# Kernel optimization log

Hardware: AMD Instinct MI355X
Metric: run time of the kernel (lower is better)

Reference implementation:

```python
import jax, jax.numpy as jnp
import numpy as np

N_NODES = 100000
N_EDGES = 1600000
F_IN = 128
D_OUT = 64
BN_EPS = 1e-3  # keras BatchNormalization default epsilon
LRELU_SLOPE = 0.2  # tf.nn.leaky_relu default alpha


def setup_inputs() -> dict:
    key = jax.random.key(0)
    ks = jax.random.split(key, 6)
    x = jax.random.normal(ks[0], (N_NODES, F_IN), dtype=jnp.float32)
    src = jax.random.randint(ks[1], (N_EDGES,), 0, N_NODES, dtype=jnp.int32)
    dst = jax.random.randint(ks[2], (N_EDGES,), 0, N_NODES, dtype=jnp.int32)
    adj_vals = jnp.ones((N_EDGES,), dtype=jnp.float32)
    W = jax.random.normal(ks[3], (F_IN, D_OUT), dtype=jnp.float32)
    K1 = jax.random.normal(ks[4], (F_IN, F_IN), dtype=jnp.float32)
    K2 = jax.random.normal(ks[5], (F_IN, F_IN), dtype=jnp.float32)
    return {"x": x, "src": src, "dst": dst, "adj_vals": adj_vals, "W": W, "K1": K1, "K2": K2}


def reference(x, src, dst, adj_vals, W, K1, K2):
    n = x.shape[0]
    # training-mode batch norm over the node (batch) axis, gamma=1, beta=0
    mean = jnp.mean(x, axis=0)
    var = jnp.var(x, axis=0)
    xn = (x - mean) * jax.lax.rsqrt(var + BN_EPS)
    mapped = xn @ W                                   # [N, D]
    a1 = jnp.tanh(jnp.sum((xn @ K1) * xn, axis=1))    # [N] row scalar
    a2 = jnp.tanh(jnp.sum((xn @ K2) * xn, axis=1))    # [N] col scalar
    # edge score e_ij = leaky_relu(v_ij*a1[i] + v_ij*a2[j])
    e = jax.nn.leaky_relu(adj_vals * (a1[src] + a2[dst]), negative_slope=LRELU_SLOPE)
    # per-row (src) sparse softmax
    emax = jax.ops.segment_max(e, src, num_segments=n)
    ee = jnp.exp(e - emax[src])
    denom = jax.ops.segment_sum(ee, src, num_segments=n)
    attn = ee / denom[src]                            # [E]
    # SpMM: out[i] = sum_j attn_ij * mapped[j]
    out = jax.ops.segment_sum(attn[:, None] * mapped[dst], src, num_segments=n)
    return jnp.tanh(out)
```

## Files before the change

### kernel.cpp

```cpp
#include <hip/hip_runtime.h>
#include <hip/hip_fp16.h>
#include <math.h>

#define F_IN 128
#define D_OUT 64
#define LRELU 0.2f
#define BN_EPS 1e-3f
#define XPITCH 136
#define NB 391
#define CHA 2048
#define CAPB 6144

typedef __attribute__((ext_vector_type(8))) __bf16 bf16x8;
typedef __attribute__((ext_vector_type(4))) __bf16 bf16x4;
typedef __attribute__((ext_vector_type(4))) float f32x4;

__global__ __launch_bounds__(256) void stats_kernel(const float* __restrict__ x,
                                                    float* __restrict__ sum,
                                                    float* __restrict__ sumsq,
                                                    int N, int rowsPerBlock) {
    __shared__ float lsum[8][132], lsq[8][132];
    int tid  = threadIdx.x;
    int c4   = (tid & 31) * 4;
    int rgrp = tid >> 5;
    int rbeg = blockIdx.x * rowsPerBlock;
    int rend = min(rbeg + rowsPerBlock, N);
    float sx = 0.f, sy = 0.f, sz = 0.f, sw = 0.f;
    float qx = 0.f, qy = 0.f, qz = 0.f, qw = 0.f;
    for (int r = rbeg + rgrp; r < rend; r += 8) {
        float4 v = *(const float4*)&x[(size_t)r * F_IN + c4];
        sx += v.x; sy += v.y; sz += v.z; sw += v.w;
        qx += v.x * v.x; qy += v.y * v.y; qz += v.z * v.z; qw += v.w * v.w;
    }
    lsum[rgrp][c4] = sx; lsum[rgrp][c4 + 1] = sy;
    lsum[rgrp][c4 + 2] = sz; lsum[rgrp][c4 + 3] = sw;
    lsq[rgrp][c4] = qx; lsq[rgrp][c4 + 1] = qy;
    lsq[rgrp][c4 + 2] = qz; lsq[rgrp][c4 + 3] = qw;
    __syncthreads();
    if (tid < 128) {
        float a = 0.f, b = 0.f;
#pragma unroll
        for (int g = 0; g < 8; ++g) { a += lsum[g][tid]; b += lsq[g][tid]; }
        atomicAdd(&sum[tid], a);
        atomicAdd(&sumsq[tid], b);
    }
}

__global__ void finalize_stats(float* sum, float* sumsq, int N) {
    int c = threadIdx.x;
    float mean = sum[c] / (float)N;
    float var  = sumsq[c] / (float)N - mean * mean;
    sum[c]   = mean;
    sumsq[c] = rsqrtf(var + BN_EPS);
}

__global__ __launch_bounds__(256) void prep_B(const float* __restrict__ K1,
                                              const float* __restrict__ K2,
                                              const float* __restrict__ W,
                                              __bf16* __restrict__ Bth,
                                              __bf16* __restrict__ Btl) {
    int i = blockIdx.x * 256 + threadIdx.x;
    if (i >= 320 * 128) return;
    int c = i >> 7, k = i & 127;
    float v;
    if (c < 128)      v = K1[k * 128 + c];
    else if (c < 256) v = K2[k * 128 + (c - 128)];
    else              v = W[k * 64 + (c - 256)];
    __bf16 h = (__bf16)v;
    int ct = c >> 4, col16 = c & 15;
    int ks = k >> 5, quad = (k >> 3) & 3, e = k & 7;
    int off = ct * 2048 + ks * 512 + (quad * 16 + col16) * 8 + e;
    Bth[off] = h;
    Btl[off] = (__bf16)(v - (float)h);
}

__global__ __launch_bounds__(256, 2) void node_kernel(const float* __restrict__ x,
                                                      const __bf16* __restrict__ Bth,
                                                      const __bf16* __restrict__ Btl,
                                                      const float* __restrict__ meanv,
                                                      const float* __restrict__ rstdv,
                                                      float* __restrict__ a1,
                                                      float* __restrict__ a2,
                                                      __half* __restrict__ mapped,
                                                      int N) {
    __shared__ __bf16 xh[64][XPITCH];
    __shared__ __bf16 xl[64][XPITCH];
    __shared__ float mS[128], rS[128];
    __shared__ float paA[4][64], paB[4][64];

    int tid   = threadIdx.x;
    int lane  = tid & 63;
    int w     = tid >> 6;
    int col16 = lane & 15;
    int quad  = lane >> 4;
    int kb    = quad * 8;

    if (tid < 128) { mS[tid] = meanv[tid]; rS[tid] = rstdv[tid]; }
    __syncthreads();

    int base = blockIdx.x * 64;

#pragma unroll
    for (int it = 0; it < 8; ++it) {
        int chunk = tid + it * 256;
        int r = chunk >> 5, c4 = (chunk & 31) * 4;
        int row = base + r;
        float f0 = 0.f, f1 = 0.f, f2 = 0.f, f3 = 0.f;
        if (row < N) {
            float4 v  = *(const float4*)&x[(size_t)row * F_IN + c4];
            float4 m  = *(const float4*)&mS[c4];
            float4 rs = *(const float4*)&rS[c4];
            f0 = (v.x - m.x) * rs.x; f1 = (v.y - m.y) * rs.y;
            f2 = (v.z - m.z) * rs.z; f3 = (v.w - m.w) * rs.w;
        }
        __bf16 h0 = (__bf16)f0, h1 = (__bf16)f1, h2 = (__bf16)f2, h3 = (__bf16)f3;
        bf16x4 hv = {h0, h1, h2, h3};
        bf16x4 lv = {(__bf16)(f0 - (float)h0), (__bf16)(f1 - (float)h1),
                     (__bf16)(f2 - (float)h2), (__bf16)(f3 - (float)h3)};
        *(bf16x4*)&xh[r][c4] = hv;
        *(bf16x4*)&xl[r][c4] = lv;
    }
    __syncthreads();

    float pa1[4] = {0, 0, 0, 0}, pa2[4] = {0, 0, 0, 0};

#pragma unroll
    for (int i = 0; i < 5; ++i) {
        int ct = w * 5 + i;
        const __bf16* ph = Bth + ct * 2048 + lane * 8;
        const __bf16* pl = Btl + ct * 2048 + lane * 8;
        bf16x8 Bh[4], Bl[4];
#pragma unroll
        for (int ks = 0; ks < 4; ++ks) {
            Bh[ks] = *(const bf16x8*)(ph + ks * 512);
            Bl[ks] = *(const bf16x8*)(pl + ks * 512);
        }
        bool isK  = (ct < 16);
        bool isA1 = (ct < 8);
        int cg = (ct & 7) * 16 + quad * 4;
        int cw = (ct - 16) * 16 + quad * 4;
#pragma unroll
        for (int rt = 0; rt < 4; ++rt) {
            int arow = rt * 16 + col16;
            bf16x8 Ah[4], Al[4];
#pragma unroll
            for (int ks = 0; ks < 4; ++ks) {
                Ah[ks] = *(bf16x8*)&xh[arow][ks * 32 + kb];
                Al[ks] = *(bf16x8*)&xl[arow][ks * 32 + kb];
            }
            f32x4 accA = {0, 0, 0, 0}, accB = {0, 0, 0, 0}, accC = {0, 0, 0, 0};
#pragma unroll
            for (int ks = 0; ks < 4; ++ks) {
                accA = __builtin_amdgcn_mfma_f32_16x16x32_bf16(Bh[ks], Ah[ks], accA, 0, 0, 0);
                accB = __builtin_amdgcn_mfma_f32_16x16x32_bf16(Bh[ks], Al[ks], accB, 0, 0, 0);
                accC = __builtin_amdgcn_mfma_f32_16x16x32_bf16(Bl[ks], Ah[ks], accC, 0, 0, 0);
            }
            f32x4 accT = accA + accB + accC;
            if (isK) {
                bf16x4 xh4 = *(bf16x4*)&xh[arow][cg];
                bf16x4 xl4 = *(bf16x4*)&xl[arow][cg];
                float s = accT[0] * ((float)xh4[0] + (float)xl4[0])
                        + accT[1] * ((float)xh4[1] + (float)xl4[1])
                        + accT[2] * ((float)xh4[2] + (float)xl4[2])
                        + accT[3] * ((float)xh4[3] + (float)xl4[3]);
                if (isA1) pa1[rt] += s; else pa2[rt] += s;
            } else {
                int node = base + arow;
                if (node < N) {
                    __half2 h01 = __floats2half2_rn(accT[0], accT[1]);
                    __half2 h23 = __floats2half2_rn(accT[2], accT[3]);
                    __half2* mp = (__half2*)&mapped[(size_t)node * 64 + cw];
                    mp[0] = h01; mp[1] = h23;
                }
            }
        }
    }

#pragma unroll
    for (int rt = 0; rt < 4; ++rt) {
        float v1 = pa1[rt], v2 = pa2[rt];
        v1 += __shfl_xor(v1, 16, 64); v1 += __shfl_xor(v1, 32, 64);
        v2 += __shfl_xor(v2, 16, 64); v2 += __shfl_xor(v2, 32, 64);
        if (quad == 0) {
            paA[w][rt * 16 + col16] = v1;
            paB[w][rt * 16 + col16] = v2;
        }
    }
    __syncthreads();
    if (tid < 64) {
        int node = base + tid;
        if (node < N) {
            a1[node] = tanhf(paA[0][tid] + paA[1][tid] + paA[2][tid] + paA[3][tid]);
            a2[node] = tanhf(paB[0][tid] + paB[1][tid] + paB[2][tid] + paB[3][tid]);
        }
    }
}

__global__ __launch_bounds__(256) void bhist_kernel(const int* __restrict__ src,
                                                    int* __restrict__ partial, int E) {
    __shared__ int h[NB];
    for (int b = threadIdx.x; b < NB; b += 256) h[b] = 0;
    __syncthreads();
    int beg = blockIdx.x * CHA;
    int end = min(beg + CHA, E);
    for (int e = beg + threadIdx.x; e < end; e += 256)
        atomicAdd(&h[src[e] >> 8], 1);
    __syncthreads();
    for (int b = threadIdx.x; b < NB; b += 256)
        partial[blockIdx.x * NB + b] = h[b];
}

__global__ __launch_bounds__(256) void bscan2_kernel(const int* __restrict__ partial,
                                                     int* __restrict__ baseT,
                                                     int* __restrict__ btot,
                                                     int nblkA) {
    __shared__ int tsum[256];
    int b   = blockIdx.x;
    int tid = threadIdx.x;
    int per = (nblkA + 255) / 256;
    int lv[8];
    int r0 = tid * per;
    int mysum = 0;
    for (int i = 0; i < per; ++i) {
        int r = r0 + i;
        lv[i] = (r < nblkA) ? partial[r * NB + b] : 0;
        mysum += lv[i];
    }
    tsum[tid] = mysum;
    for (int off = 1; off < 256; off <<= 1) {
        __syncthreads();
        int t = (tid >= off) ? tsum[tid - off] : 0;
        __syncthreads();
        tsum[tid] += t;
    }
    __syncthreads();
    int run = tsum[tid] - mysum;
    for (int i = 0; i < per; ++i) {
        int r = r0 + i;
        if (r < nblkA) { baseT[r * NB + b] = run; run += lv[i]; }
    }
    if (tid == 255) btot[b] = tsum[255];
}

__global__ __launch_bounds__(512) void bscan_kernel(const int* __restrict__ btot,
                                                    int* __restrict__ bscan,
                                                    int* __restrict__ rowptr,
                                                    int N, int E) {
    __shared__ int s[512];
    int b = threadIdx.x;
    int v = (b < NB) ? btot[b] : 0;
    s[b] = v;
    for (int off = 1; off < 512; off <<= 1) {
        __syncthreads();
        int t = (b >= off) ? s[b - off] : 0;
        __syncthreads();
        s[b] += t;
    }
    __syncthreads();
    if (b < NB) bscan[b] = s[b] - v;
    if (b == 0) { bscan[NB] = E; rowptr[N] = E; }
}

__global__ __launch_bounds__(256) void binA_kernel(const int* __restrict__ src,
                                                   const int* __restrict__ dst,
                                                   const float* __restrict__ adj,
                                                   const float* __restrict__ a1,
                                                   const float* __restrict__ a2,
                                                   const int* __restrict__ partial,
                                                   const int* __restrict__ baseT,
                                                   const int* __restrict__ bscan,
                                                   int2* __restrict__ sorted, int E) {
    __shared__ int2 listL[CHA];
    __shared__ int  addrL[CHA];
    __shared__ int  scan0[NB], scanW[NB], curL[NB];
    __shared__ int  tsum[256];
    int tid = threadIdx.x;
    int blk = blockIdx.x;
    int ebase = blk * CHA;
    int count = min(CHA, E - ebase);

    int b0 = tid * 2, b1 = tid * 2 + 1;
    int v0 = (b0 < NB) ? partial[blk * NB + b0] : 0;
    int v1 = (b1 < NB) ? partial[blk * NB + b1] : 0;
    tsum[tid] = v0 + v1;
    for (int off = 1; off < 256; off <<= 1) {
        __syncthreads();
        int t = (tid >= off) ? tsum[tid - off] : 0;
        __syncthreads();
        tsum[tid] += t;
    }
    __syncthreads();
    int excl = tsum[tid] - v0 - v1;
    if (b0 < NB) {
        scan0[b0] = excl; scanW[b0] = excl;
        curL[b0] = baseT[blk * NB + b0] + bscan[b0];
    }
    if (b1 < NB) {
        scan0[b1] = excl + v0; scanW[b1] = excl + v0;
        curL[b1] = baseT[blk * NB + b1] + bscan[b1];
    }
    __syncthreads();

    for (int i = tid; i < count; i += 256) {
        int e = ebase + i;
        int s = src[e], d = dst[e];
        float v = adj[e] * (a1[s] + a2[d]);
        v = (v > 0.f) ? v : LRELU * v;
        float ex = __expf(v);
        int b = s >> 8;
        int p = atomicAdd(&scanW[b], 1);
        listL[p] = make_int2(((s & 255) << 24) | d, __float_as_int(ex));
        addrL[p] = curL[b] + (p - scan0[b]);
    }
    __syncthreads();
    for (int i = tid; i < count; i += 256)
        sorted[addrL[i]] = listL[i];
}

__global__ __launch_bounds__(256) void binB_kernel(const int* __restrict__ bscan,
                                                   int2* __restrict__ sorted,
                                                   int* __restrict__ rowptr, int N) {
    __shared__ int2 inL[CAPB];
    __shared__ int2 outL[CAPB];
    __shared__ int  c0[257], cW[256];
    int b   = blockIdx.x;
    int lo  = b << 8;
    int bbase = bscan[b];
    int len   = bscan[b + 1] - bbase;
    len = min(len, CAPB);
    int tid = threadIdx.x;
    cW[tid] = 0;
    __syncthreads();
    for (int i = tid; i < len; i += 256) {
        int2 pe = sorted[bbase + i];
        inL[i] = pe;
        atomicAdd(&cW[((unsigned)pe.x) >> 24], 1);
    }
    __syncthreads();
    if (tid == 0) {
        int run = 0;
        for (int k = 0; k < 256; ++k) { int c = cW[k]; c0[k] = run; run += c; }
    }
    __syncthreads();
    if (lo + tid < N) rowptr[lo + tid] = bbase + c0[tid];
    cW[tid] = c0[tid];
    __syncthreads();
    for (int i = tid; i < len; i += 256) {
        int2 pe = inL[i];
        unsigned u = (unsigned)pe.x;
        int p = atomicAdd(&cW[u >> 24], 1);
        outL[p] = make_int2((int)(u & 0xFFFFFF), pe.y);
    }
    __syncthreads();
    for (int i = tid; i < len; i += 256)
        sorted[bbase + i] = outL[i];
}

#define SPMM_ACC(P, G)                                        \
    {                                                         \
        float wg = __int_as_float(P.y);                       \
        accw += wg;                                           \
        float2 m0 = __half22float2(*(__half2*)&G.x);          \
        float2 m1 = __half22float2(*(__half2*)&G.y);          \
        float2 m2 = __half22float2(*(__half2*)&G.z);          \
        float2 m3 = __half22float2(*(__half2*)&G.w);          \
        acc0 += wg * m0.x; acc1 += wg * m0.y;                 \
        acc2 += wg * m1.x; acc3 += wg * m1.y;                 \
        acc4 += wg * m2.x; acc5 += wg * m2.y;                 \
        acc6 += wg * m3.x; acc7 += wg * m3.y;                 \
    }

__global__ __launch_bounds__(256) void spmm_kernel(const int* __restrict__ rowptr,
                                                   const int2* __restrict__ sorted,
                                                   const __half2* __restrict__ mapped,
                                                   float* __restrict__ out, int N) {
    __shared__ float accL[8][64];
    __shared__ float accwL[8];
    int tid  = threadIdx.x;
    int w    = tid >> 6;
    int lane = tid & 63;
    int half = lane >> 5;
    int slot = (lane >> 3) & 3;
    int c    = lane & 7;
    int nl   = w * 2 + half;
    int node = blockIdx.x * 8 + nl;
    int beg = 0, end = 0;
    if (node < N) { beg = rowptr[node]; end = rowptr[node + 1]; }

    float acc0 = 0.f, acc1 = 0.f, acc2 = 0.f, acc3 = 0.f;
    float acc4 = 0.f, acc5 = 0.f, acc6 = 0.f, acc7 = 0.f;
    float accw = 0.f;
    const char* mb = (const char*)mapped;

    for (int chunk = beg; chunk < end; chunk += 16) {
        int e0 = chunk + slot;
        int2 p0 = (e0      < end) ? sorted[e0]      : make_int2(0, 0);
        int2 p1 = (e0 + 4  < end) ? sorted[e0 + 4]  : make_int2(0, 0);
        int2 p2 = (e0 + 8  < end) ? sorted[e0 + 8]  : make_int2(0, 0);
        int2 p3 = (e0 + 12 < end) ? sorted[e0 + 12] : make_int2(0, 0);
        int4 g0 = *(const int4*)(mb + (((unsigned)p0.x << 7) | (c << 4)));
        int4 g1 = *(const int4*)(mb + (((unsigned)p1.x << 7) | (c << 4)));
        int4 g2 = *(const int4*)(mb + (((unsigned)p2.x << 7) | (c << 4)));
        int4 g3 = *(const int4*)(mb + (((unsigned)p3.x << 7) | (c << 4)));
        SPMM_ACC(p0, g0);
        SPMM_ACC(p1, g1);
        SPMM_ACC(p2, g2);
        SPMM_ACC(p3, g3);
    }

#pragma unroll
    for (int off = 8; off < 32; off <<= 1) {
        acc0 += __shfl_xor(acc0, off, 64);
        acc1 += __shfl_xor(acc1, off, 64);
        acc2 += __shfl_xor(acc2, off, 64);
        acc3 += __shfl_xor(acc3, off, 64);
        acc4 += __shfl_xor(acc4, off, 64);
        acc5 += __shfl_xor(acc5, off, 64);
        acc6 += __shfl_xor(acc6, off, 64);
        acc7 += __shfl_xor(acc7, off, 64);
        accw += __shfl_xor(accw, off, 64);
    }
    if (slot == 0) {
        float* al = &accL[nl][c * 8];
        al[0] = acc0; al[1] = acc1; al[2] = acc2; al[3] = acc3;
        al[4] = acc4; al[5] = acc5; al[6] = acc6; al[7] = acc7;
        if (c == 0) accwL[nl] = accw;
    }
    __syncthreads();

    int n    = tid >> 5;
    int col  = tid & 31;
    int node2 = blockIdx.x * 8 + n;
    if (node2 < N) {
        float aw  = accwL[n];
        float inv = (aw != 0.f) ? 1.f / aw : 0.f;
        float* op = &out[(size_t)node2 * 64];
        op[col]      = tanhf(accL[n][col] * inv);
        op[col + 32] = tanhf(accL[n][col + 32] * inv);
    }
}

extern "C" void kernel_launch(void* const* d_in, const int* in_sizes, int n_in,
                              void* d_out, int out_size, void* d_ws, size_t ws_size,
                              hipStream_t stream) {
    const float* x   = (const float*)d_in[0];
    const int*   src = (const int*)d_in[1];
    const int*   dst = (const int*)d_in[2];
    const float* adj = (const float*)d_in[3];
    const float* W   = (const float*)d_in[4];
    const float* K1  = (const float*)d_in[5];
    const float* K2  = (const float*)d_in[6];
    float* out = (float*)d_out;

    const int N = in_sizes[0] / F_IN;
    const int E = in_sizes[1];
    const int nblkA = (E + CHA - 1) / CHA;

    float* meanv  = (float*)d_ws;
    float* rstdv  = meanv + 128;
    float* a1     = rstdv + 128;
    float* a2     = a1 + N;
    __half* mapped = (__half*)(a2 + N);
    int*   rowptr = (int*)(mapped + (size_t)N * 64);
    int*   bscan  = rowptr + (N + 1);
    int*   btot   = bscan + (NB + 1);
    int*   partial = btot + NB;
    int*   baseT   = partial + (size_t)nblkA * NB;
    uintptr_t sp  = ((uintptr_t)(baseT + (size_t)nblkA * NB) + 15) & ~(uintptr_t)15;
    int2*  sorted = (int2*)sp;
    __bf16* Bth   = (__bf16*)(sorted + E);
    __bf16* Btl   = Bth + 320 * 128;

    hipMemsetAsync(d_ws, 0, 256 * sizeof(float), stream);

    bhist_kernel<<<nblkA, 256, 0, stream>>>(src, partial, E);

    int rpb = (N + 511) / 512;
    stats_kernel<<<512, 256, 0, stream>>>(x, meanv, rstdv, N, rpb);
    finalize_stats<<<1, 128, 0, stream>>>(meanv, rstdv, N);

    prep_B<<<(320 * 128 + 255) / 256, 256, 0, stream>>>(K1, K2, W, Bth, Btl);

    node_kernel<<<(N + 63) / 64, 256, 0, stream>>>(x, Bth, Btl, meanv, rstdv,
                                                   a1, a2, mapped, N);

    bscan2_kernel<<<NB, 256, 0, stream>>>(partial, baseT, btot, nblkA);
    bscan_kernel<<<1, 512, 0, stream>>>(btot, bscan, rowptr, N, E);

    binA_kernel<<<nblkA, 256, 0, stream>>>(src, dst, adj, a1, a2,
                                           partial, baseT, bscan, sorted, E);
    binB_kernel<<<NB, 256, 0, stream>>>(bscan, sorted, rowptr, N);

    spmm_kernel<<<(N + 7) / 8, 256, 0, stream>>>(rowptr, sorted,
                                                 (const __half2*)mapped, out, N);
}
```

Measured before the change: 284.3 us.

## Double node tile to 128 rows and reuse A fragments across two column tiles

The node kernel now processes 128 nodes per block instead of 64. Each wave loads B fragments for two column tiles at once and reuses every loaded A row fragment across both, so LDS reads of A are halved and B global loads are amortized over more rows. In exchange LDS use roughly doubles to about 70KB per block and register pressure rises from the doubled B fragments and the accumulators. Occupancy may drop below the launch-bounds target of 2 blocks, and the grid has half as many blocks.

```diff
diff --git a/kernel.cpp b/kernel.cpp
--- a/kernel.cpp
+++ b/kernel.cpp
@@ -83,10 +83,10 @@
                                                       float* __restrict__ a2,
                                                       __half* __restrict__ mapped,
                                                       int N) {
-    __shared__ __bf16 xh[64][XPITCH];
-    __shared__ __bf16 xl[64][XPITCH];
+    __shared__ __bf16 xh[128][XPITCH];
+    __shared__ __bf16 xl[128][XPITCH];
     __shared__ float mS[128], rS[128];
-    __shared__ float paA[4][64], paB[4][64];
+    __shared__ float paA[4][128], paB[4][128];
 
     int tid   = threadIdx.x;
     int lane  = tid & 63;
@@ -98,10 +98,10 @@
     if (tid < 128) { mS[tid] = meanv[tid]; rS[tid] = rstdv[tid]; }
     __syncthreads();
 
-    int base = blockIdx.x * 64;
-
-#pragma unroll
-    for (int it = 0; it < 8; ++it) {
+    int base = blockIdx.x * 128;
+
+#pragma unroll
+    for (int it = 0; it < 16; ++it) {
         int chunk = tid + it * 256;
         int r = chunk >> 5, c4 = (chunk & 31) * 4;
         int row = base + r;
@@ -122,25 +122,29 @@
     }
     __syncthreads();
 
-    float pa1[4] = {0, 0, 0, 0}, pa2[4] = {0, 0, 0, 0};
-
-#pragma unroll
-    for (int i = 0; i < 5; ++i) {
-        int ct = w * 5 + i;
-        const __bf16* ph = Bth + ct * 2048 + lane * 8;
-        const __bf16* pl = Btl + ct * 2048 + lane * 8;
-        bf16x8 Bh[4], Bl[4];
-#pragma unroll
-        for (int ks = 0; ks < 4; ++ks) {
-            Bh[ks] = *(const bf16x8*)(ph + ks * 512);
-            Bl[ks] = *(const bf16x8*)(pl + ks * 512);
+    float pa1[8] = {0, 0, 0, 0, 0, 0, 0, 0};
+    float pa2[8] = {0, 0, 0, 0, 0, 0, 0, 0};
+
+#pragma unroll
+    for (int g = 0; g < 3; ++g) {
+        int t0 = g * 2;
+        int gn = (g < 2) ? 2 : 1;
+        bf16x8 Bh[2][4], Bl[2][4];
+#pragma unroll
+        for (int t = 0; t < 2; ++t) {
+            if (t < gn) {
+                int ct = w * 5 + t0 + t;
+                const __bf16* ph = Bth + ct * 2048 + lane * 8;
+                const __bf16* pl = Btl + ct * 2048 + lane * 8;
+#pragma unroll
+                for (int ks = 0; ks < 4; ++ks) {
+                    Bh[t][ks] = *(const bf16x8*)(ph + ks * 512);
+                    Bl[t][ks] = *(const bf16x8*)(pl + ks * 512);
+                }
+            }
         }
-        bool isK  = (ct < 16);
-        bool isA1 = (ct < 8);
-        int cg = (ct & 7) * 16 + quad * 4;
-        int cw = (ct - 16) * 16 + quad * 4;
-#pragma unroll
-        for (int rt = 0; rt < 4; ++rt) {
+#pragma unroll
+        for (int rt = 0; rt < 8; ++rt) {
             int arow = rt * 16 + col16;
             bf16x8 Ah[4], Al[4];
 #pragma unroll
@@ -148,36 +152,45 @@
                 Ah[ks] = *(bf16x8*)&xh[arow][ks * 32 + kb];
                 Al[ks] = *(bf16x8*)&xl[arow][ks * 32 + kb];
             }
-            f32x4 accA = {0, 0, 0, 0}, accB = {0, 0, 0, 0}, accC = {0, 0, 0, 0};
-#pragma unroll
-            for (int ks = 0; ks < 4; ++ks) {
-                accA = __builtin_amdgcn_mfma_f32_16x16x32_bf16(Bh[ks], Ah[ks], accA, 0, 0, 0);
-                accB = __builtin_amdgcn_mfma_f32_16x16x32_bf16(Bh[ks], Al[ks], accB, 0, 0, 0);
-                accC = __builtin_amdgcn_mfma_f32_16x16x32_bf16(Bl[ks], Ah[ks], accC, 0, 0, 0);
-            }
-            f32x4 accT = accA + accB + accC;
-            if (isK) {
-                bf16x4 xh4 = *(bf16x4*)&xh[arow][cg];
-                bf16x4 xl4 = *(bf16x4*)&xl[arow][cg];
-                float s = accT[0] * ((float)xh4[0] + (float)xl4[0])
-                        + accT[1] * ((float)xh4[1] + (float)xl4[1])
-                        + accT[2] * ((float)xh4[2] + (float)xl4[2])
-                        + accT[3] * ((float)xh4[3] + (float)xl4[3]);
-                if (isA1) pa1[rt] += s; else pa2[rt] += s;
-            } else {
-                int node = base + arow;
-                if (node < N) {
-                    __half2 h01 = __floats2half2_rn(accT[0], accT[1]);
-                    __half2 h23 = __floats2half2_rn(accT[2], accT[3]);
-                    __half2* mp = (__half2*)&mapped[(size_t)node * 64 + cw];
-                    mp[0] = h01; mp[1] = h23;
+#pragma unroll
+            for (int t = 0; t < 2; ++t) {
+                if (t >= gn) continue;
+                int ct = w * 5 + t0 + t;
+                bool isK  = (ct < 16);
+                bool isA1 = (ct < 8);
+                int cg = (ct & 7) * 16 + quad * 4;
+                int cw = (ct - 16) * 16 + quad * 4;
+                f32x4 accA = {0, 0, 0, 0}, accB = {0, 0, 0, 0}, accC = {0, 0, 0, 0};
+#pragma unroll
+                for (int ks = 0; ks < 4; ++ks) {
+                    accA = __builtin_amdgcn_mfma_f32_16x16x32_bf16(Bh[t][ks], Ah[ks], accA, 0, 0, 0);
+                    accB = __builtin_amdgcn_mfma_f32_16x16x32_bf16(Bh[t][ks], Al[ks], accB, 0, 0, 0);
+                    accC = __builtin_amdgcn_mfma_f32_16x16x32_bf16(Bl[t][ks], Ah[ks], accC, 0, 0, 0);
+                }
+                f32x4 accT = accA + accB + accC;
+                if (isK) {
+                    bf16x4 xh4 = *(bf16x4*)&xh[arow][cg];
+                    bf16x4 xl4 = *(bf16x4*)&xl[arow][cg];
+                    float s = accT[0] * ((float)xh4[0] + (float)xl4[0])
+                            + accT[1] * ((float)xh4[1] + (float)xl4[1])
+                            + accT[2] * ((float)xh4[2] + (float)xl4[2])
+                            + accT[3] * ((float)xh4[3] + (float)xl4[3]);
+                    if (isA1) pa1[rt] += s; else pa2[rt] += s;
+                } else {
+                    int node = base + arow;
+                    if (node < N) {
+                        __half2 h01 = __floats2half2_rn(accT[0], accT[1]);
+                        __half2 h23 = __floats2half2_rn(accT[2], accT[3]);
+                        __half2* mp = (__half2*)&mapped[(size_t)node * 64 + cw];
+                        mp[0] = h01; mp[1] = h23;
+                    }
                 }
             }
         }
     }
 
 #pragma unroll
-    for (int rt = 0; rt < 4; ++rt) {
+    for (int rt = 0; rt < 8; ++rt) {
         float v1 = pa1[rt], v2 = pa2[rt];
         v1 += __shfl_xor(v1, 16, 64); v1 += __shfl_xor(v1, 32, 64);
         v2 += __shfl_xor(v2, 16, 64); v2 += __shfl_xor(v2, 32, 64);
@@ -187,7 +200,7 @@
         }
     }
     __syncthreads();
-    if (tid < 64) {
+    if (tid < 128) {
         int node = base + tid;
         if (node < N) {
             a1[node] = tanhf(paA[0][tid] + paA[1][tid] + paA[2][tid] + paA[3][tid]);
@@ -481,8 +494,8 @@
 
     prep_B<<<(320 * 128 + 255) / 256, 256, 0, stream>>>(K1, K2, W, Bth, Btl);
 
-    node_kernel<<<(N + 63) / 64, 256, 0, stream>>>(x, Bth, Btl, meanv, rstdv,
-                                                   a1, a2, mapped, N);
+    node_kernel<<<(N + 127) / 128, 256, 0, stream>>>(x, Bth, Btl, meanv, rstdv,
+                                                     a1, a2, mapped, N);
 
     bscan2_kernel<<<NB, 256, 0, stream>>>(partial, baseT, btot, nblkA);
     bscan_kernel<<<1, 512, 0, stream>>>(btot, bscan, rowptr, N, E);
```

Measured after the change: 370.8 us. 1.3x slower.
